# Performance work log

Hardware: AMD Instinct MI355X
Metric: run time of the kernel (lower is better)

Reference implementation:

```python
import jax, jax.numpy as jnp
import numpy as np

N_NODES = 100_000
N_EDGES = 1_600_000
D_IN = 64
D_OUT = 64


def setup_inputs() -> dict:
    key = jax.random.key(0)
    k1, k2, k3, k4, k5, k6, k7, k8 = jax.random.split(key, 8)
    edge_row = jax.random.randint(k1, (N_EDGES,), 0, N_NODES, dtype=jnp.int32)
    edge_col = jax.random.randint(k2, (N_EDGES,), 0, N_NODES, dtype=jnp.int32)
    # normalized adjacency values (e.g. sym-normalized weights)
    edge_vals = jax.random.uniform(k3, (N_EDGES,), dtype=jnp.float32)
    node_feat = jax.random.normal(k4, (N_NODES, D_IN), dtype=jnp.float32)
    scale = (6.0 / (D_IN + D_OUT)) ** 0.5  # xavier_uniform
    W1 = jax.random.uniform(k5, (D_IN, D_OUT), minval=-scale, maxval=scale, dtype=jnp.float32)
    W2 = jax.random.uniform(k6, (D_IN, D_OUT), minval=-scale, maxval=scale, dtype=jnp.float32)
    b1 = jax.random.normal(k7, (D_OUT,), dtype=jnp.float32) * 0.02
    b2 = jax.random.normal(k8, (D_OUT,), dtype=jnp.float32) * 0.02
    return {"edge_row": edge_row, "edge_col": edge_col, "edge_vals": edge_vals,
            "node_feat": node_feat, "W1": W1, "b1": b1, "W2": W2, "b2": b2}


def reference(edge_row, edge_col, edge_vals, node_feat, W1, b1, W2, b2):
    # agg = sparse.mm(mat, node_feat): gather neighbor feats, weight, scatter-add
    gathered = edge_vals[:, None] * node_feat[edge_col]          # [E, D_IN]
    agg_feat = jax.ops.segment_sum(gathered, edge_row, num_segments=N_NODES)  # [N, D_IN]
    leaky = lambda x: jnp.where(x >= 0, x, 0.2 * x)
    part1 = leaky(agg_feat @ W1 + b1)                            # [N, D_OUT]
    part2 = leaky((agg_feat * node_feat) @ W2 + b2)              # [N, D_OUT]
    # dropout is identity in eval mode
    return part1 + part2
```

## Files before the change

### kernel.cpp

```cpp
#include <hip/hip_runtime.h>

#define NN 100000
#define NE 1600000
#define D 64
#define NB 256
#define EPB (NE / NB)
#define BROWS 128
#define HROWS 64
#define NBK ((NN + BROWS - 1) / BROWS)
#define NH (NBK * NB)
#define SCAN_BLK 1024
#define NSB ((NH + SCAN_BLK - 1) / SCAN_BLK)
#define CAP 1536
#define WT_LD 72

static constexpr size_t OFF_AGG16  = 0;
static constexpr size_t OFF_BH     = 12800000;
static constexpr size_t OFF_BS     = 13600768;
static constexpr size_t OFF_COARSE = 13601792;
static constexpr size_t OFF_F16    = 26401792;

typedef short bf16x8 __attribute__((ext_vector_type(8)));
typedef float f32x4 __attribute__((ext_vector_type(4)));

__device__ __forceinline__ unsigned short f32_to_bf16_rn(float x) {
    unsigned int u = __float_as_uint(x);
    u += 0x7FFFu + ((u >> 16) & 1u);
    return (unsigned short)(u >> 16);
}
__device__ __forceinline__ float bf16_to_f32(unsigned int lo16) {
    return __uint_as_float(lo16 << 16);
}

__global__ __launch_bounds__(256) void conv_k(const float* __restrict__ feat,
                                              unsigned short* __restrict__ feat16) {
    int i = blockIdx.x * blockDim.x + threadIdx.x;
    if (i >= NN * D / 8) return;
    const float4 f0 = *reinterpret_cast<const float4*>(&feat[i * 8]);
    const float4 f1 = *reinterpret_cast<const float4*>(&feat[i * 8 + 4]);
    uint4 o;
    o.x = f32_to_bf16_rn(f0.x) | ((unsigned int)f32_to_bf16_rn(f0.y) << 16);
    o.y = f32_to_bf16_rn(f0.z) | ((unsigned int)f32_to_bf16_rn(f0.w) << 16);
    o.z = f32_to_bf16_rn(f1.x) | ((unsigned int)f32_to_bf16_rn(f1.y) << 16);
    o.w = f32_to_bf16_rn(f1.z) | ((unsigned int)f32_to_bf16_rn(f1.w) << 16);
    *reinterpret_cast<uint4*>(&feat16[i * 8]) = o;
}

__global__ __launch_bounds__(256) void bhist_k(const int* __restrict__ rows,
                                               int* __restrict__ bh) {
    __shared__ int h[NBK];
    for (int i = threadIdx.x; i < NBK; i += 256) h[i] = 0;
    __syncthreads();
    const int e0 = blockIdx.x * EPB;
    for (int e = e0 + threadIdx.x; e < e0 + EPB; e += 256)
        atomicAdd(&h[rows[e] >> 7], 1);
    __syncthreads();
    for (int i = threadIdx.x; i < NBK; i += 256) bh[i * NB + blockIdx.x] = h[i];
}

__global__ __launch_bounds__(256) void scan1_k(int* __restrict__ a,
                                               int* __restrict__ bsum) {
    __shared__ int tsum[256];
    const int base = blockIdx.x * SCAN_BLK + threadIdx.x * 4;
    int v[4];
    int s = 0;
#pragma unroll
    for (int i = 0; i < 4; ++i) {
        int idx = base + i;
        v[i] = (idx < NH) ? a[idx] : 0;
        s += v[i];
    }
    tsum[threadIdx.x] = s;
    __syncthreads();
    int x = s;
    for (int off = 1; off < 256; off <<= 1) {
        int y = (threadIdx.x >= off) ? tsum[threadIdx.x - off] : 0;
        __syncthreads();
        x += y;
        tsum[threadIdx.x] = x;
        __syncthreads();
    }
    int run = x - s;
#pragma unroll
    for (int i = 0; i < 4; ++i) {
        int idx = base + i;
        if (idx < NH) a[idx] = run;
        run += v[i];
    }
    if (threadIdx.x == 255) bsum[blockIdx.x] = x;
}

__global__ void scan2_k(int* __restrict__ bsum) {
    __shared__ int s[256];
    int i = threadIdx.x;
    int v = (i < NSB) ? bsum[i] : 0;
    s[i] = v;
    __syncthreads();
    int x = v;
    for (int off = 1; off < 256; off <<= 1) {
        int y = (i >= off) ? s[i - off] : 0;
        __syncthreads();
        x += y;
        s[i] = x;
        __syncthreads();
    }
    if (i < NSB) bsum[i] = x - v;
}

__global__ __launch_bounds__(256) void scan3_k(int* __restrict__ a,
                                               const int* __restrict__ bsum) {
    int i = blockIdx.x * blockDim.x + threadIdx.x;
    if (i < NH) a[i] += bsum[i >> 10];
}

__global__ __launch_bounds__(256) void bin_k(const int* __restrict__ rows,
                                             const int* __restrict__ cols,
                                             const float* __restrict__ vals,
                                             const int* __restrict__ bh,
                                             int2* __restrict__ coarse) {
    __shared__ int cur[NBK];
    for (int i = threadIdx.x; i < NBK; i += 256) cur[i] = 0;
    __syncthreads();
    const int e0 = blockIdx.x * EPB;
    for (int e = e0 + threadIdx.x; e < e0 + EPB; e += 256) {
        int r = rows[e];
        int b = r >> 7;
        int pos = atomicAdd(&cur[b], 1);
        coarse[bh[b * NB + blockIdx.x] + pos] =
            make_int2(((r & 127) << 17) | cols[e], __float_as_int(vals[e]));
    }
}

__global__ __launch_bounds__(256) void bgather_k(const int* __restrict__ bh,
                                                 const int2* __restrict__ coarse,
                                                 const unsigned short* __restrict__ feat16,
                                                 unsigned short* __restrict__ agg16) {
    __shared__ int2 se[CAP];
    __shared__ int hist[HROWS];
    __shared__ int rsl[HROWS];
    const int blk = blockIdx.x;
    const int b = blk >> 1;
    const int h = blk & 1;
    const int start = bh[b * NB];
    const int end = (b == NBK - 1) ? NE : bh[(b + 1) * NB];

    const int tid = threadIdx.x;
    if (tid < HROWS) hist[tid] = 0;
    __syncthreads();
    for (int i = start + tid; i < end; i += 256) {
        int rl = ((unsigned)coarse[i].x) >> 17;
        if ((rl >> 6) == h) atomicAdd(&hist[rl & 63], 1);
    }
    __syncthreads();
    if (tid < HROWS) rsl[tid] = hist[tid];
    __syncthreads();
    for (int off = 1; off < HROWS; off <<= 1) {
        int y = 0;
        if (tid < HROWS && tid >= off) y = rsl[tid - off];
        __syncthreads();
        if (tid < HROWS) rsl[tid] += y;
        __syncthreads();
    }
    if (tid < HROWS) hist[tid] = rsl[tid] - hist[tid];
    __syncthreads();
    for (int i = start + tid; i < end; i += 256) {
        int2 ev = coarse[i];
        int rl = ((unsigned)ev.x) >> 17;
        if ((rl >> 6) == h) {
            int p = atomicAdd(&hist[rl & 63], 1);
            if (p < CAP) se[p] = ev;
        }
    }
    __syncthreads();

    const int lane = tid & 63;
    const int wv = tid >> 6;
    const int g = lane >> 3;
    const int t = lane & 7;
    const int rowbase = b * BROWS + h * HROWS;

    for (int rl = wv * 16; rl < wv * 16 + 16; ++rl) {
        int r0 = (rl == 0) ? 0 : rsl[rl - 1];
        int r1 = rsl[rl];
        if (r0 > CAP) r0 = CAP;
        if (r1 > CAP) r1 = CAP;
        float acc[8];
#pragma unroll
        for (int k = 0; k < 8; ++k) acc[k] = 0.f;
        for (int base2 = r0; base2 < r1; base2 += 8) {
            int m = r1 - base2;
            if (m > 8) m = 8;
            int2 ev = se[base2 + (g < m ? g : 0)];
            float vj = (g < m) ? __int_as_float(ev.y) : 0.f;
            int cj = ev.x & 0x1FFFF;
            const uint4 f =
                *reinterpret_cast<const uint4*>(&feat16[(size_t)cj * D + (t << 3)]);
            acc[0] += vj * bf16_to_f32(f.x & 0xffffu);
            acc[1] += vj * bf16_to_f32(f.x >> 16);
            acc[2] += vj * bf16_to_f32(f.y & 0xffffu);
            acc[3] += vj * bf16_to_f32(f.y >> 16);
            acc[4] += vj * bf16_to_f32(f.z & 0xffffu);
            acc[5] += vj * bf16_to_f32(f.z >> 16);
            acc[6] += vj * bf16_to_f32(f.w & 0xffffu);
            acc[7] += vj * bf16_to_f32(f.w >> 16);
        }
#pragma unroll
        for (int off = 8; off <= 32; off <<= 1) {
#pragma unroll
            for (int k = 0; k < 8; ++k) acc[k] += __shfl_xor(acc[k], off);
        }
        const int r = rowbase + rl;
        if (lane < 8 && r < NN) {
            uint4 o;
            o.x = f32_to_bf16_rn(acc[0]) | ((unsigned int)f32_to_bf16_rn(acc[1]) << 16);
            o.y = f32_to_bf16_rn(acc[2]) | ((unsigned int)f32_to_bf16_rn(acc[3]) << 16);
            o.z = f32_to_bf16_rn(acc[4]) | ((unsigned int)f32_to_bf16_rn(acc[5]) << 16);
            o.w = f32_to_bf16_rn(acc[6]) | ((unsigned int)f32_to_bf16_rn(acc[7]) << 16);
            *reinterpret_cast<uint4*>(&agg16[(size_t)r * D + (t << 3)]) = o;
        }
    }
}

__global__ __launch_bounds__(256) void mlp_k(const unsigned short* __restrict__ agg16,
                                             const unsigned short* __restrict__ feat16,
                                             const float* __restrict__ W1,
                                             const float* __restrict__ b1,
                                             const float* __restrict__ W2,
                                             const float* __restrict__ b2,
                                             float* __restrict__ out) {
    __shared__ unsigned short W1t[64 * WT_LD];
    __shared__ unsigned short W2t[64 * WT_LD];
    for (int idx = threadIdx.x; idx < 4096; idx += 256) {
        int k = idx >> 6, n = idx & 63;
        W1t[n * WT_LD + k] = f32_to_bf16_rn(W1[idx]);
        W2t[n * WT_LD + k] = f32_to_bf16_rn(W2[idx]);
    }
    __syncthreads();

    const int lane = threadIdx.x & 63;
    const int wv = threadIdx.x >> 6;
    const int lm = lane & 15;
    const int lk = lane >> 4;
    const int rowA = blockIdx.x * 64 + wv * 16 + lm;
    const bool valid = rowA < NN;
    const size_t abase = (size_t)rowA * D;

    f32x4 acc1[4], acc2[4];
#pragma unroll
    for (int nb = 0; nb < 4; ++nb) {
        acc1[nb] = (f32x4){0.f, 0.f, 0.f, 0.f};
        acc2[nb] = (f32x4){0.f, 0.f, 0.f, 0.f};
    }

    union U { uint4 u; bf16x8 v; };

#pragma unroll
    for (int kk = 0; kk < 2; ++kk) {
        const int k0 = kk * 32 + lk * 8;
        U ua, uf, um;
        ua.u = make_uint4(0, 0, 0, 0);
        uf.u = make_uint4(0, 0, 0, 0);
        if (valid) {
            ua.u = *reinterpret_cast<const uint4*>(&agg16[abase + k0]);
            uf.u = *reinterpret_cast<const uint4*>(&feat16[abase + k0]);
        }
        {
            const unsigned int* au = &ua.u.x;
            const unsigned int* fu = &uf.u.x;
            unsigned int* mu = &um.u.x;
#pragma unroll
            for (int q = 0; q < 4; ++q) {
                float lo = bf16_to_f32(au[q] & 0xffffu) * bf16_to_f32(fu[q] & 0xffffu);
                float hi = bf16_to_f32(au[q] >> 16) * bf16_to_f32(fu[q] >> 16);
                mu[q] = f32_to_bf16_rn(lo) | ((unsigned int)f32_to_bf16_rn(hi) << 16);
            }
        }
#pragma unroll
        for (int nb = 0; nb < 4; ++nb) {
            U b1f, b2f;
            b1f.v = *reinterpret_cast<const bf16x8*>(&W1t[(nb * 16 + lm) * WT_LD + k0]);
            b2f.v = *reinterpret_cast<const bf16x8*>(&W2t[(nb * 16 + lm) * WT_LD + k0]);
            acc1[nb] = __builtin_amdgcn_mfma_f32_16x16x32_bf16(ua.v, b1f.v, acc1[nb], 0, 0, 0);
            acc2[nb] = __builtin_amdgcn_mfma_f32_16x16x32_bf16(um.v, b2f.v, acc2[nb], 0, 0, 0);
        }
    }

#pragma unroll
    for (int nb = 0; nb < 4; ++nb) {
        const int col = nb * 16 + lm;
        const float bb1 = b1[col];
        const float bb2 = b2[col];
#pragma unroll
        for (int j = 0; j < 4; ++j) {
            const int row = blockIdx.x * 64 + wv * 16 + lk * 4 + j;
            if (row < NN) {
                float x1 = acc1[nb][j] + bb1;
                float x2 = acc2[nb][j] + bb2;
                x1 = x1 >= 0.f ? x1 : 0.2f * x1;
                x2 = x2 >= 0.f ? x2 : 0.2f * x2;
                out[(size_t)row * D + col] = x1 + x2;
            }
        }
    }
}

extern "C" void kernel_launch(void* const* d_in, const int* in_sizes, int n_in,
                              void* d_out, int out_size, void* d_ws, size_t ws_size,
                              hipStream_t stream) {
    const int* rows = (const int*)d_in[0];
    const int* cols = (const int*)d_in[1];
    const float* vals = (const float*)d_in[2];
    const float* feat = (const float*)d_in[3];
    const float* W1 = (const float*)d_in[4];
    const float* b1 = (const float*)d_in[5];
    const float* W2 = (const float*)d_in[6];
    const float* b2 = (const float*)d_in[7];
    float* out = (float*)d_out;

    char* ws = (char*)d_ws;
    unsigned short* agg16 = (unsigned short*)(ws + OFF_AGG16);
    int* bh = (int*)(ws + OFF_BH);
    int* bsum = (int*)(ws + OFF_BS);
    int2* coarse = (int2*)(ws + OFF_COARSE);
    unsigned short* feat16 = (unsigned short*)(ws + OFF_F16);

    conv_k<<<(NN * D / 8 + 255) / 256, 256, 0, stream>>>(feat, feat16);

    bhist_k<<<NB, 256, 0, stream>>>(rows, bh);
    scan1_k<<<NSB, 256, 0, stream>>>(bh, bsum);
    scan2_k<<<1, 256, 0, stream>>>(bsum);
    scan3_k<<<(NH + 255) / 256, 256, 0, stream>>>(bh, bsum);
    bin_k<<<NB, 256, 0, stream>>>(rows, cols, vals, bh, coarse);

    bgather_k<<<NBK * 2, 256, 0, stream>>>(bh, coarse, feat16, agg16);

    const int ntiles = (NN + 63) / 64;
    mlp_k<<<ntiles, 256, 0, stream>>>(agg16, feat16, W1, b1, W2, b2, out);
}
```

Measured before the change: 116.7 us.

## Split edge records into keys and bf16 values, fold scan fixup, batch gather indices

Binned edges are now stored as a 32-bit key array plus a separate bf16 value array instead of int2 pairs, which cuts binning write and read traffic. The scan3 fixup kernel is removed; consumers add the block prefix themselves, which saves a launch. The number of binning blocks doubles, so scan2 now runs with 512 threads. In the gather loop each lane loads one edge from LDS and the indices are then broadcast through shuffles. Storing edge weights in bf16 loses precision.

```diff
diff --git a/kernel.cpp b/kernel.cpp
--- a/kernel.cpp
+++ b/kernel.cpp
@@ -3,7 +3,7 @@
 #define NN 100000
 #define NE 1600000
 #define D 64
-#define NB 256
+#define NB 512
 #define EPB (NE / NB)
 #define BROWS 128
 #define HROWS 64
@@ -14,11 +14,12 @@
 #define CAP 1536
 #define WT_LD 72
 
-static constexpr size_t OFF_AGG16  = 0;
-static constexpr size_t OFF_BH     = 12800000;
-static constexpr size_t OFF_BS     = 13600768;
-static constexpr size_t OFF_COARSE = 13601792;
-static constexpr size_t OFF_F16    = 26401792;
+static constexpr size_t OFF_AGG16 = 0;
+static constexpr size_t OFF_BH    = 12800000;
+static constexpr size_t OFF_BS    = 14401536;
+static constexpr size_t OFF_KEYS  = 14403584;
+static constexpr size_t OFF_VALS  = 20803584;
+static constexpr size_t OFF_F16   = 24003584;
 
 typedef short bf16x8 __attribute__((ext_vector_type(8)));
 typedef float f32x4 __attribute__((ext_vector_type(4)));
@@ -91,13 +92,13 @@
 }
 
 __global__ void scan2_k(int* __restrict__ bsum) {
-    __shared__ int s[256];
+    __shared__ int s[512];
     int i = threadIdx.x;
     int v = (i < NSB) ? bsum[i] : 0;
     s[i] = v;
     __syncthreads();
     int x = v;
-    for (int off = 1; off < 256; off <<= 1) {
+    for (int off = 1; off < 512; off <<= 1) {
         int y = (i >= off) ? s[i - off] : 0;
         __syncthreads();
         x += y;
@@ -105,50 +106,54 @@
         __syncthreads();
     }
     if (i < NSB) bsum[i] = x - v;
-}
-
-__global__ __launch_bounds__(256) void scan3_k(int* __restrict__ a,
-                                               const int* __restrict__ bsum) {
-    int i = blockIdx.x * blockDim.x + threadIdx.x;
-    if (i < NH) a[i] += bsum[i >> 10];
 }
 
 __global__ __launch_bounds__(256) void bin_k(const int* __restrict__ rows,
                                              const int* __restrict__ cols,
                                              const float* __restrict__ vals,
                                              const int* __restrict__ bh,
-                                             int2* __restrict__ coarse) {
+                                             const int* __restrict__ bsum,
+                                             int* __restrict__ keys,
+                                             unsigned short* __restrict__ vals16) {
     __shared__ int cur[NBK];
-    for (int i = threadIdx.x; i < NBK; i += 256) cur[i] = 0;
+    for (int i = threadIdx.x; i < NBK; i += 256) {
+        int idx = i * NB + blockIdx.x;
+        cur[i] = bh[idx] + bsum[idx >> 10];
+    }
     __syncthreads();
     const int e0 = blockIdx.x * EPB;
     for (int e = e0 + threadIdx.x; e < e0 + EPB; e += 256) {
         int r = rows[e];
         int b = r >> 7;
-        int pos = atomicAdd(&cur[b], 1);
-        coarse[bh[b * NB + blockIdx.x] + pos] =
-            make_int2(((r & 127) << 17) | cols[e], __float_as_int(vals[e]));
+        int p = atomicAdd(&cur[b], 1);
+        keys[p] = ((r & 127) << 17) | cols[e];
+        vals16[p] = f32_to_bf16_rn(vals[e]);
     }
 }
 
 __global__ __launch_bounds__(256) void bgather_k(const int* __restrict__ bh,
-                                                 const int2* __restrict__ coarse,
+                                                 const int* __restrict__ bsum,
+                                                 const int* __restrict__ keys,
+                                                 const unsigned short* __restrict__ vals16,
                                                  const unsigned short* __restrict__ feat16,
                                                  unsigned short* __restrict__ agg16) {
-    __shared__ int2 se[CAP];
+    __shared__ int sek[CAP];
+    __shared__ unsigned short sev[CAP];
     __shared__ int hist[HROWS];
     __shared__ int rsl[HROWS];
     const int blk = blockIdx.x;
     const int b = blk >> 1;
     const int h = blk & 1;
-    const int start = bh[b * NB];
-    const int end = (b == NBK - 1) ? NE : bh[(b + 1) * NB];
+    const int i0 = b * NB;
+    const int i1 = (b + 1) * NB;
+    const int start = bh[i0] + bsum[i0 >> 10];
+    const int end = (b == NBK - 1) ? NE : (bh[i1] + bsum[i1 >> 10]);
 
     const int tid = threadIdx.x;
     if (tid < HROWS) hist[tid] = 0;
     __syncthreads();
     for (int i = start + tid; i < end; i += 256) {
-        int rl = ((unsigned)coarse[i].x) >> 17;
+        int rl = ((unsigned)keys[i]) >> 17;
         if ((rl >> 6) == h) atomicAdd(&hist[rl & 63], 1);
     }
     __syncthreads();
@@ -164,11 +169,14 @@
     if (tid < HROWS) hist[tid] = rsl[tid] - hist[tid];
     __syncthreads();
     for (int i = start + tid; i < end; i += 256) {
-        int2 ev = coarse[i];
-        int rl = ((unsigned)ev.x) >> 17;
+        int kv = keys[i];
+        int rl = ((unsigned)kv) >> 17;
         if ((rl >> 6) == h) {
             int p = atomicAdd(&hist[rl & 63], 1);
-            if (p < CAP) se[p] = ev;
+            if (p < CAP) {
+                sek[p] = kv;
+                sev[p] = vals16[i];
+            }
         }
     }
     __syncthreads();
@@ -187,22 +195,31 @@
         float acc[8];
 #pragma unroll
         for (int k = 0; k < 8; ++k) acc[k] = 0.f;
-        for (int base2 = r0; base2 < r1; base2 += 8) {
-            int m = r1 - base2;
-            if (m > 8) m = 8;
-            int2 ev = se[base2 + (g < m ? g : 0)];
-            float vj = (g < m) ? __int_as_float(ev.y) : 0.f;
-            int cj = ev.x & 0x1FFFF;
-            const uint4 f =
-                *reinterpret_cast<const uint4*>(&feat16[(size_t)cj * D + (t << 3)]);
-            acc[0] += vj * bf16_to_f32(f.x & 0xffffu);
-            acc[1] += vj * bf16_to_f32(f.x >> 16);
-            acc[2] += vj * bf16_to_f32(f.y & 0xffffu);
-            acc[3] += vj * bf16_to_f32(f.y >> 16);
-            acc[4] += vj * bf16_to_f32(f.z & 0xffffu);
-            acc[5] += vj * bf16_to_f32(f.z >> 16);
-            acc[6] += vj * bf16_to_f32(f.w & 0xffffu);
-            acc[7] += vj * bf16_to_f32(f.w >> 16);
+        for (int base2 = r0; base2 < r1; base2 += 64) {
+            int nn = r1 - base2;
+            if (nn > 64) nn = 64;
+            int c = 0;
+            float v = 0.f;
+            if (lane < nn) {
+                c = sek[base2 + lane] & 0x1FFFF;
+                v = bf16_to_f32((unsigned)sev[base2 + lane]);
+            }
+            const int niter = (nn + 7) >> 3;
+            for (int jj = 0; jj < niter; ++jj) {
+                int src = (jj << 3) + g;
+                int cj = __shfl(c, src);
+                float vj = __shfl(v, src);
+                const uint4 f =
+                    *reinterpret_cast<const uint4*>(&feat16[(size_t)cj * D + (t << 3)]);
+                acc[0] += vj * bf16_to_f32(f.x & 0xffffu);
+                acc[1] += vj * bf16_to_f32(f.x >> 16);
+                acc[2] += vj * bf16_to_f32(f.y & 0xffffu);
+                acc[3] += vj * bf16_to_f32(f.y >> 16);
+                acc[4] += vj * bf16_to_f32(f.z & 0xffffu);
+                acc[5] += vj * bf16_to_f32(f.z >> 16);
+                acc[6] += vj * bf16_to_f32(f.w & 0xffffu);
+                acc[7] += vj * bf16_to_f32(f.w >> 16);
+            }
         }
 #pragma unroll
         for (int off = 8; off <= 32; off <<= 1) {
@@ -321,18 +338,18 @@
     unsigned short* agg16 = (unsigned short*)(ws + OFF_AGG16);
     int* bh = (int*)(ws + OFF_BH);
     int* bsum = (int*)(ws + OFF_BS);
-    int2* coarse = (int2*)(ws + OFF_COARSE);
+    int* keys = (int*)(ws + OFF_KEYS);
+    unsigned short* vals16 = (unsigned short*)(ws + OFF_VALS);
     unsigned short* feat16 = (unsigned short*)(ws + OFF_F16);
 
     conv_k<<<(NN * D / 8 + 255) / 256, 256, 0, stream>>>(feat, feat16);
 
     bhist_k<<<NB, 256, 0, stream>>>(rows, bh);
     scan1_k<<<NSB, 256, 0, stream>>>(bh, bsum);
-    scan2_k<<<1, 256, 0, stream>>>(bsum);
-    scan3_k<<<(NH + 255) / 256, 256, 0, stream>>>(bh, bsum);
-    bin_k<<<NB, 256, 0, stream>>>(rows, cols, vals, bh, coarse);
-
-    bgather_k<<<NBK * 2, 256, 0, stream>>>(bh, coarse, feat16, agg16);
+    scan2_k<<<1, 512, 0, stream>>>(bsum);
+    bin_k<<<NB, 256, 0, stream>>>(rows, cols, vals, bh, bsum, keys, vals16);
+
+    bgather_k<<<NBK * 2, 256, 0, stream>>>(bh, bsum, keys, vals16, feat16, agg16);
 
     const int ntiles = (NN + 63) / 64;
     mlp_k<<<ntiles, 256, 0, stream>>>(agg16, feat16, W1, b1, W2, b2, out);
```

New measurement: 138.9 us. +19.0%, slower.
